# Kernel tuning notes

Hardware: AMD Instinct MI355X
Metric: run time of the kernel (lower is better)

Reference implementation:

```python
import jax, jax.numpy as jnp
import numpy as np

BETA = 0.25

def _encoder(x, W0, b0, W1, b1, W2, b2):
    # MLP: Linear+ReLU, Linear+ReLU, Linear (dims 768->512->256->64)
    h = jax.nn.relu(x @ W0 + b0)
    h = jax.nn.relu(h @ W1 + b1)
    return h @ W2 + b2

def _rvq(z, codebooks):
    # Residual vector quantization over L=4 levels (structurally distinct loop).
    residual = z
    x_q = jnp.zeros_like(z)
    losses = []
    codes = []
    for l in range(codebooks.shape[0]):
        cb = codebooks[l]  # [K, e]
        # squared L2 distances [N, K] via expansion (avoids materializing [N,K,e])
        d = (jnp.sum(residual * residual, axis=1, keepdims=True)
             - 2.0 * residual @ cb.T
             + jnp.sum(cb * cb, axis=1))
        idx = jnp.argmin(d, axis=1)           # [N]
        q = cb[idx]                            # gather [N, e]
        # codebook loss + beta * commitment loss
        loss = (jnp.mean((jax.lax.stop_gradient(q) - residual) ** 2)
                + BETA * jnp.mean((q - jax.lax.stop_gradient(residual)) ** 2))
        losses.append(loss)
        # straight-through estimator
        q_st = residual + jax.lax.stop_gradient(q - residual)
        residual = residual - q_st
        x_q = x_q + q_st
        codes.append(idx)
    rq_loss = jnp.mean(jnp.stack(losses))
    return x_q, rq_loss, jnp.stack(codes)  # codes: [L, N] int


def setup_inputs() -> dict:
    key = jax.random.key(0)
    ks = jax.random.split(key, 8)
    N, D = 131072, 768
    dims = [768, 512, 256, 64]
    x = jax.random.normal(ks[0], (N, D), dtype=jnp.float32)
    W0 = jax.random.normal(ks[1], (dims[0], dims[1]), dtype=jnp.float32) * (1.0 / np.sqrt(dims[0]))
    b0 = jnp.zeros((dims[1],), dtype=jnp.float32)
    W1 = jax.random.normal(ks[2], (dims[1], dims[2]), dtype=jnp.float32) * (1.0 / np.sqrt(dims[1]))
    b1 = jnp.zeros((dims[2],), dtype=jnp.float32)
    W2 = jax.random.normal(ks[3], (dims[2], dims[3]), dtype=jnp.float32) * (1.0 / np.sqrt(dims[2]))
    b2 = jnp.zeros((dims[3],), dtype=jnp.float32)
    codebooks = jax.random.normal(ks[4], (4, 256, 64), dtype=jnp.float32)
    return {"x": x, "W0": W0, "b0": b0, "W1": W1, "b1": b1, "W2": W2, "b2": b2,
            "codebooks": codebooks}


def reference(x, W0, b0, W1, b1, W2, b2, codebooks):
    z = _encoder(x, W0, b0, W1, b1, W2, b2)          # [N, 64]
    x_q, rq_loss, codes = _rvq(z, codebooks)
    return x_q, rq_loss, codes
```

## Files before the change

### kernel.cpp

```cpp
#include <hip/hip_runtime.h>
#include <hip/hip_bf16.h>


typedef double d2v __attribute__((ext_vector_type(2)));

template<bool RELU>
__global__ __launch_bounds__(256) void gemm128(
    const float* __restrict__ A, const float* __restrict__ W,
    const float* __restrict__ bias, float* __restrict__ C,
    int M, int N, int K)
{
    __shared__ float As[16][132];
    __shared__ float Bs[16][132];

    const int tid = threadIdx.x;
    const int tx = tid & 15;
    const int ty = tid >> 4;
    const int col0 = blockIdx.x * 128;
    const int row0 = blockIdx.y * 128;

    const float* Ab = A + (size_t)row0 * K;
    const float* Wb = W + col0;

    const int am0 = tid >> 2,          ak0 = (tid & 3) * 4;
    const int am1 = (tid + 256) >> 2,  ak1 = ((tid + 256) & 3) * 4;
    const int bk0 = tid >> 5,          bn0 = (tid & 31) * 4;
    const int bk1 = (tid + 256) >> 5,  bn1 = ((tid + 256) & 31) * 4;

    float acc[8][8] = {};

    float4 sa0 = *reinterpret_cast<const float4*>(Ab + (size_t)am0 * K + ak0);
    float4 sa1 = *reinterpret_cast<const float4*>(Ab + (size_t)am1 * K + ak1);
    float4 sb0 = *reinterpret_cast<const float4*>(Wb + (size_t)bk0 * N + bn0);
    float4 sb1 = *reinterpret_cast<const float4*>(Wb + (size_t)bk1 * N + bn1);
    As[ak0 + 0][am0] = sa0.x; As[ak0 + 1][am0] = sa0.y;
    As[ak0 + 2][am0] = sa0.z; As[ak0 + 3][am0] = sa0.w;
    As[ak1 + 0][am1] = sa1.x; As[ak1 + 1][am1] = sa1.y;
    As[ak1 + 2][am1] = sa1.z; As[ak1 + 3][am1] = sa1.w;
    *reinterpret_cast<float4*>(&Bs[bk0][bn0]) = sb0;
    *reinterpret_cast<float4*>(&Bs[bk1][bn1]) = sb1;
    __syncthreads();

    for (int k0 = 0; k0 < K; k0 += 16) {
        const bool hasNext = (k0 + 16 < K);
        if (hasNext) {
            const float* An = Ab + k0 + 16;
            const float* Wn = Wb + (size_t)(k0 + 16) * N;
            sa0 = *reinterpret_cast<const float4*>(An + (size_t)am0 * K + ak0);
            sa1 = *reinterpret_cast<const float4*>(An + (size_t)am1 * K + ak1);
            sb0 = *reinterpret_cast<const float4*>(Wn + (size_t)bk0 * N + bn0);
            sb1 = *reinterpret_cast<const float4*>(Wn + (size_t)bk1 * N + bn1);
        }

#pragma unroll
        for (int kk = 0; kk < 16; ++kk) {
            float4 a0 = *reinterpret_cast<const float4*>(&As[kk][ty * 4]);
            float4 a1 = *reinterpret_cast<const float4*>(&As[kk][64 + ty * 4]);
            float4 b0 = *reinterpret_cast<const float4*>(&Bs[kk][tx * 4]);
            float4 b1 = *reinterpret_cast<const float4*>(&Bs[kk][64 + tx * 4]);
            float ar[8] = {a0.x, a0.y, a0.z, a0.w, a1.x, a1.y, a1.z, a1.w};
            float br[8] = {b0.x, b0.y, b0.z, b0.w, b1.x, b1.y, b1.z, b1.w};
#pragma unroll
            for (int m = 0; m < 8; ++m)
#pragma unroll
                for (int n = 0; n < 8; ++n)
                    acc[m][n] = fmaf(ar[m], br[n], acc[m][n]);
        }

        if (hasNext) {
            __syncthreads();
            As[ak0 + 0][am0] = sa0.x; As[ak0 + 1][am0] = sa0.y;
            As[ak0 + 2][am0] = sa0.z; As[ak0 + 3][am0] = sa0.w;
            As[ak1 + 0][am1] = sa1.x; As[ak1 + 1][am1] = sa1.y;
            As[ak1 + 2][am1] = sa1.z; As[ak1 + 3][am1] = sa1.w;
            *reinterpret_cast<float4*>(&Bs[bk0][bn0]) = sb0;
            *reinterpret_cast<float4*>(&Bs[bk1][bn1]) = sb1;
            __syncthreads();
        }
    }

    float bl[4], bh[4];
#pragma unroll
    for (int n = 0; n < 4; ++n) {
        bl[n] = bias[col0 + tx * 4 + n];
        bh[n] = bias[col0 + 64 + tx * 4 + n];
    }
#pragma unroll
    for (int half = 0; half < 2; ++half) {
#pragma unroll
        for (int r = 0; r < 4; ++r) {
            int m = half * 4 + r;
            int row = row0 + half * 64 + ty * 4 + r;
            float4 lo, hi;
            lo.x = acc[m][0] + bl[0]; lo.y = acc[m][1] + bl[1];
            lo.z = acc[m][2] + bl[2]; lo.w = acc[m][3] + bl[3];
            hi.x = acc[m][4] + bh[0]; hi.y = acc[m][5] + bh[1];
            hi.z = acc[m][6] + bh[2]; hi.w = acc[m][7] + bh[3];
            if (RELU) {
                lo.x = fmaxf(lo.x, 0.f); lo.y = fmaxf(lo.y, 0.f);
                lo.z = fmaxf(lo.z, 0.f); lo.w = fmaxf(lo.w, 0.f);
                hi.x = fmaxf(hi.x, 0.f); hi.y = fmaxf(hi.y, 0.f);
                hi.z = fmaxf(hi.z, 0.f); hi.w = fmaxf(hi.w, 0.f);
            }
            float* Cr = C + (size_t)row * N + col0;
            *reinterpret_cast<float4*>(Cr + tx * 4) = lo;
            *reinterpret_cast<float4*>(Cr + 64 + tx * 4) = hi;
        }
    }
}

template<bool RELU>
__global__ __launch_bounds__(256) void gemm_bias(
    const float* __restrict__ A, const float* __restrict__ W,
    const float* __restrict__ bias, float* __restrict__ C,
    int M, int N, int K)
{
    __shared__ float As[16][132];
    __shared__ float Bs[16][68];

    const int tid = threadIdx.x;
    const int tx = tid & 15;
    const int ty = tid >> 4;
    const int col0 = blockIdx.x * 64;
    const int row0 = blockIdx.y * 128;

    const float* Ab = A + (size_t)row0 * K;
    const float* Wb = W + col0;

    float acc[8][4] = {};

    for (int k0 = 0; k0 < K; k0 += 16) {
#pragma unroll
        for (int i = 0; i < 2; ++i) {
            int pos = tid + i * 256;
            int m  = pos >> 2;
            int k4 = (pos & 3) * 4;
            float4 v = *reinterpret_cast<const float4*>(Ab + (size_t)m * K + k0 + k4);
            As[k4 + 0][m] = v.x; As[k4 + 1][m] = v.y;
            As[k4 + 2][m] = v.z; As[k4 + 3][m] = v.w;
        }
        {
            int kk = tid >> 4;
            int n4 = (tid & 15) * 4;
            float4 v = *reinterpret_cast<const float4*>(Wb + (size_t)(k0 + kk) * N + n4);
            *reinterpret_cast<float4*>(&Bs[kk][n4]) = v;
        }
        __syncthreads();
#pragma unroll
        for (int kk = 0; kk < 16; ++kk) {
            float4 a0 = *reinterpret_cast<const float4*>(&As[kk][ty * 8]);
            float4 a1 = *reinterpret_cast<const float4*>(&As[kk][ty * 8 + 4]);
            float4 bv = *reinterpret_cast<const float4*>(&Bs[kk][tx * 4]);
            float a[8] = {a0.x, a0.y, a0.z, a0.w, a1.x, a1.y, a1.z, a1.w};
            float b[4] = {bv.x, bv.y, bv.z, bv.w};
#pragma unroll
            for (int m = 0; m < 8; ++m)
#pragma unroll
                for (int n = 0; n < 4; ++n)
                    acc[m][n] = fmaf(a[m], b[n], acc[m][n]);
        }
        __syncthreads();
    }

    float bv[4];
#pragma unroll
    for (int n = 0; n < 4; ++n) bv[n] = bias[col0 + tx * 4 + n];
#pragma unroll
    for (int m = 0; m < 8; ++m) {
        int row = row0 + ty * 8 + m;
        float4 o;
        float v0 = acc[m][0] + bv[0];
        float v1 = acc[m][1] + bv[1];
        float v2 = acc[m][2] + bv[2];
        float v3 = acc[m][3] + bv[3];
        if (RELU) {
            v0 = fmaxf(v0, 0.f); v1 = fmaxf(v1, 0.f);
            v2 = fmaxf(v2, 0.f); v3 = fmaxf(v3, 0.f);
        }
        o.x = v0; o.y = v1; o.z = v2; o.w = v3;
        *reinterpret_cast<float4*>(C + (size_t)row * N + col0 + tx * 4) = o;
    }
}

__global__ void cb_norms(const float* __restrict__ cb,
                         double* __restrict__ cn64, float* __restrict__ cnf) {
    int c = blockIdx.x * 64 + threadIdx.x;
    const float* p = cb + (size_t)c * 64;
    double s = 0.0;
#pragma unroll
    for (int j = 0; j < 64; ++j) {
        double v = (double)p[j];
        s = fma(v, v, s);
    }
    cn64[c] = s;
    cnf[c]  = (float)s;
}

__global__ void build_cbw(const float* __restrict__ cb, double* __restrict__ cbw) {
    int i = blockIdx.x * 256 + threadIdx.x;
    cbw[i] = -2.0 * (double)cb[i];
}

#define EGUARD 1e-3

__device__ __forceinline__ double rank64(const double* __restrict__ p,
                                         double R0, const float (&rd)[64]) {
    double c0 = 0.0, c1 = 0.0, c2 = 0.0, c3 = 0.0;
#pragma unroll
    for (int j = 0; j < 16; ++j) {
        d2v x = *reinterpret_cast<const d2v*>(p + j * 4);
        d2v y = *reinterpret_cast<const d2v*>(p + j * 4 + 2);
        c0 = fma(x[0], (double)rd[j * 4 + 0], c0);
        c1 = fma(x[1], (double)rd[j * 4 + 1], c1);
        c2 = fma(y[0], (double)rd[j * 4 + 2], c2);
        c3 = fma(y[1], (double)rd[j * 4 + 3], c3);
    }
    return R0 + ((c0 + c1) + (c2 + c3));
}

__global__ __launch_bounds__(256, 2) void rvq_v5(
    const float* __restrict__ z,
    const float* __restrict__ cbf,
    const double* __restrict__ cbw,
    const double* __restrict__ cn64,
    const float* __restrict__ cnf,
    float* __restrict__ xq,
    float* __restrict__ codes,
    double* __restrict__ partials,
    int row0, int Ntot)
{
    __shared__ float sd1[4][64];
    __shared__ float sd2[4][64];
    __shared__ int   si1[4][64];
    __shared__ int   si2[4][64];

    const int tid  = threadIdx.x;
    const int lane = tid & 63;
    const int w    = tid >> 6;
    const int wu   = __builtin_amdgcn_readfirstlane(w);
    const int blk  = blockIdx.x;
    const int grow0 = row0 + blk * 64;

    float rd[64];
    const float* zr = z + (size_t)(blk * 64 + lane) * 64;
#pragma unroll
    for (int q = 0; q < 16; ++q) {
        float4 v = *reinterpret_cast<const float4*>(zr + q * 4);
        rd[q * 4 + 0] = v.x; rd[q * 4 + 1] = v.y;
        rd[q * 4 + 2] = v.z; rd[q * 4 + 3] = v.w;
    }

    double sse = 0.0;

    for (int lv = 0; lv < 4; ++lv) {
        const int cbase = lv * 256;
        __syncthreads();

        const float* cwl = cbf + (size_t)(cbase + wu * 64) * 64;
        const float* cnl = cnf + cbase + wu * 64;

        float d1 = 3.4e38f, d2 = 3.4e38f;
        int   i1 = 0,       i2 = 0;

#pragma unroll 1
        for (int c = 0; c < 64; ++c) {
            const float* cp = cwl + c * 64;
            float acc8[8];
#pragma unroll
            for (int q = 0; q < 8; ++q) {
                float4 va = *reinterpret_cast<const float4*>(cp + q * 8);
                float4 vb = *reinterpret_cast<const float4*>(cp + q * 8 + 4);
                float t = 0.f;
                t = fmaf(va.x, rd[q * 8 + 0], t);
                t = fmaf(va.y, rd[q * 8 + 1], t);
                t = fmaf(va.z, rd[q * 8 + 2], t);
                t = fmaf(va.w, rd[q * 8 + 3], t);
                t = fmaf(vb.x, rd[q * 8 + 4], t);
                t = fmaf(vb.y, rd[q * 8 + 5], t);
                t = fmaf(vb.z, rd[q * 8 + 6], t);
                t = fmaf(vb.w, rd[q * 8 + 7], t);
                acc8[q] = t;
            }
            float dot = ((acc8[0] + acc8[1]) + (acc8[2] + acc8[3]))
                      + ((acc8[4] + acc8[5]) + (acc8[6] + acc8[7]));
            float d = fmaf(-2.f, dot, cnl[c]);
            int code = wu * 64 + c;
            if (d < d1) { d2 = d1; i2 = i1; d1 = d; i1 = code; }
            else if (d < d2) { d2 = d; i2 = code; }
        }

        sd1[w][lane] = d1; si1[w][lane] = i1;
        sd2[w][lane] = d2; si2[w][lane] = i2;
        __syncthreads();

        float bd1 = sd1[0][lane]; int bi1 = si1[0][lane]; int wstar = 0;
#pragma unroll
        for (int ww = 1; ww < 4; ++ww) {
            float dd = sd1[ww][lane]; int ii = si1[ww][lane];
            if (dd < bd1 || (dd == bd1 && ii < bi1)) { bd1 = dd; bi1 = ii; wstar = ww; }
        }
        float d2g = 3.4e38f; int i2g = 0;
#pragma unroll
        for (int ww = 0; ww < 4; ++ww) {
            float dd = (ww == wstar) ? sd2[ww][lane] : sd1[ww][lane];
            int   ii = (ww == wstar) ? si2[ww][lane] : si1[ww][lane];
            if (dd < d2g) { d2g = dd; i2g = ii; }
        }

        double R1 = rank64(cbw + (size_t)(cbase + bi1) * 64, cn64[cbase + bi1], rd);
        double R2 = rank64(cbw + (size_t)(cbase + i2g) * 64, cn64[cbase + i2g], rd);
        int ci; double Rw;
        if (R1 < R2 || (R1 == R2 && bi1 < i2g)) { ci = bi1; Rw = R1; }
        else                                    { ci = i2g; Rw = R2; }

        if (!(Rw < (double)d2g - EGUARD)) {
            float l8f = fminf(fminf(sd2[0][lane], sd2[1][lane]),
                              fminf(sd2[2][lane], sd2[3][lane]));
            double L8 = (double)l8f;
            double Rm = 1.0e300; int im = 0;
#pragma unroll
            for (int ww = 0; ww < 4; ++ww) {
#pragma unroll
                for (int k = 0; k < 2; ++k) {
                    int cc = k ? si2[ww][lane] : si1[ww][lane];
                    double R = rank64(cbw + (size_t)(cbase + cc) * 64,
                                      cn64[cbase + cc], rd);
                    if (R < Rm || (R == Rm && cc < im)) { Rm = R; im = cc; }
                }
            }
            if (Rm < L8 - EGUARD) {
                ci = im;
            } else {
                double dmin = 1.0e300; int imin = 0;
#pragma unroll 1
                for (int c = 0; c < 256; ++c) {
                    double R = rank64(cbw + (size_t)(cbase + c) * 64,
                                      cn64[cbase + c], rd);
                    if (R < dmin) { dmin = R; imin = c; }
                }
                ci = imin;
            }
        }

        const float* qp = cbf + (size_t)(cbase + ci) * 64;
        double lsse = 0.0;
#pragma unroll
        for (int q = 0; q < 16; ++q) {
            float4 qv = *reinterpret_cast<const float4*>(qp + q * 4);
            float r0 = rd[q * 4 + 0], r1 = rd[q * 4 + 1];
            float r2 = rd[q * 4 + 2], r3 = rd[q * 4 + 3];
            if (w == 0) {
                float e0 = qv.x - r0, e1 = qv.y - r1;
                float e2 = qv.z - r2, e3 = qv.w - r3;
                lsse = fma((double)e0, (double)e0, lsse);
                lsse = fma((double)e1, (double)e1, lsse);
                lsse = fma((double)e2, (double)e2, lsse);
                lsse = fma((double)e3, (double)e3, lsse);
            }
            rd[q * 4 + 0] = r0 - qv.x; rd[q * 4 + 1] = r1 - qv.y;
            rd[q * 4 + 2] = r2 - qv.z; rd[q * 4 + 3] = r3 - qv.w;
        }
        if (w == 0) {
            sse += lsse;
            codes[(size_t)lv * Ntot + grow0 + lane] = (float)ci;
        }
    }

    if (w == 0) {
        size_t base = (size_t)(grow0 + lane) * 64;
#pragma unroll
        for (int q = 0; q < 16; ++q) {
            float4 zv = *reinterpret_cast<const float4*>(zr + q * 4);
            float4 o;
            o.x = zv.x - rd[q * 4 + 0];
            o.y = zv.y - rd[q * 4 + 1];
            o.z = zv.z - rd[q * 4 + 2];
            o.w = zv.w - rd[q * 4 + 3];
            *reinterpret_cast<float4*>(xq + base + q * 4) = o;
        }
        double s = sse;
#pragma unroll
        for (int off = 32; off > 0; off >>= 1) {
            union { double d; int i[2]; } u; u.d = s;
            u.i[0] = __shfl_down(u.i[0], off, 64);
            u.i[1] = __shfl_down(u.i[1], off, 64);
            s += u.d;
        }
        if (lane == 0) partials[grow0 >> 6] = s;
    }
}

__global__ void loss_final(const double* __restrict__ partials, int n,
                           float* __restrict__ out, double scale) {
    __shared__ double s[256];
    double acc = 0.0;
    for (int i = threadIdx.x; i < n; i += 256) acc += partials[i];
    s[threadIdx.x] = acc;
    __syncthreads();
    for (int off = 128; off > 0; off >>= 1) {
        if ((int)threadIdx.x < off) s[threadIdx.x] += s[threadIdx.x + off];
        __syncthreads();
    }
    if (threadIdx.x == 0) *out = (float)(s[0] * scale);
}

extern "C" void kernel_launch(void* const* d_in, const int* in_sizes, int n_in,
                              void* d_out, int out_size, void* d_ws, size_t ws_size,
                              hipStream_t stream) {
    const float* x  = (const float*)d_in[0];
    const float* W0 = (const float*)d_in[1];
    const float* b0 = (const float*)d_in[2];
    const float* W1 = (const float*)d_in[3];
    const float* b1 = (const float*)d_in[4];
    const float* W2 = (const float*)d_in[5];
    const float* b2 = (const float*)d_in[6];
    const float* cb = (const float*)d_in[7];

    const int N = in_sizes[0] / 768;

    float* out   = (float*)d_out;
    float* xq    = out;
    float* loss  = out + (size_t)N * 64;
    float* codes = loss + 1;

    const int nblk_total = N / 64;
    const size_t tail_floats = 131072 + 2048 + 2 * (size_t)nblk_total + 1024 + 64;

    size_t avail = ws_size / 4;
    avail = (avail > tail_floats) ? (avail - tail_floats) : 0;
    int Nc = (int)(avail / 832);
    Nc = (Nc / 128) * 128;
    if (Nc > N) Nc = N;
    if (Nc < 128) Nc = 128;

    float* ws = (float*)d_ws;
    float* h0 = ws;
    float* h1 = h0 + (size_t)Nc * 512;
    float* z  = h1 + (size_t)Nc * 256;
    double* cbw      = (double*)(ws + (size_t)Nc * 832);
    double* cn64     = cbw + 65536;
    double* partials = cn64 + 1024;
    float*  cnf      = (float*)(partials + nblk_total);

    cb_norms <<<16, 64, 0, stream>>>(cb, cn64, cnf);
    build_cbw<<<256, 256, 0, stream>>>(cb, cbw);

    for (int r0 = 0; r0 < N; r0 += Nc) {
        int cur = (N - r0 < Nc) ? (N - r0) : Nc;
        gemm128<true ><<<dim3(512 / 128, cur / 128), 256, 0, stream>>>(
            x + (size_t)r0 * 768, W0, b0, h0, cur, 512, 768);
        gemm128<true ><<<dim3(256 / 128, cur / 128), 256, 0, stream>>>(
            h0, W1, b1, h1, cur, 256, 512);
        gemm_bias<false><<<dim3(1, cur / 128), 256, 0, stream>>>(
            h1, W2, b2, z, cur, 64, 256);
        rvq_v5<<<cur / 64, 256, 0, stream>>>(
            z, cb, cbw, cn64, cnf, xq, codes, partials, r0, N);
    }

    loss_final<<<1, 256, 0, stream>>>(partials, nblk_total, loss,
                                      1.25 / (4.0 * (double)N * 64.0));
}
```

Measured before the change: 2.668 ms.

## Double-buffer GEMM shared tiles, remap workgroups per XCD, relax RVQ launch bounds

The fp32 SIMT GEMM now keeps two shared-memory buffers, so the next K tile is written to the spare buffer and only one barrier per step is needed instead of two. Workgroups use a 1D grid whose block ids are remapped so that consecutive tiles land on the same XCD, which is meant to improve L2 reuse of the A rows and weight columns. The RVQ kernel drops its min-blocks-per-CU hint, giving the compiler more registers at the risk of lower occupancy. Doubling the shared tiles also raises LDS use per block.

```diff
diff --git a/kernel.cpp b/kernel.cpp
--- a/kernel.cpp
+++ b/kernel.cpp
@@ -4,20 +4,29 @@
 
 typedef double d2v __attribute__((ext_vector_type(2)));
 
-template<bool RELU>
+template<bool RELU, int NCOLSHIFT>
 __global__ __launch_bounds__(256) void gemm128(
     const float* __restrict__ A, const float* __restrict__ W,
     const float* __restrict__ bias, float* __restrict__ C,
     int M, int N, int K)
 {
-    __shared__ float As[16][132];
-    __shared__ float Bs[16][132];
+    __shared__ float As[2][16][132];
+    __shared__ float Bs[2][16][132];
+
+    const int nwg  = gridDim.x;
+    const int b    = blockIdx.x;
+    const int xcd  = b & 7;
+    const int rest = b >> 3;
+    const int q8   = nwg >> 3, r8 = nwg & 7;
+    const int wg   = (xcd < r8 ? xcd * (q8 + 1) : r8 * (q8 + 1) + (xcd - r8) * q8) + rest;
+    const int NCOL = 1 << NCOLSHIFT;
+
+    const int col0 = (wg & (NCOL - 1)) * 128;
+    const int row0 = (wg >> NCOLSHIFT) * 128;
 
     const int tid = threadIdx.x;
     const int tx = tid & 15;
     const int ty = tid >> 4;
-    const int col0 = blockIdx.x * 128;
-    const int row0 = blockIdx.y * 128;
 
     const float* Ab = A + (size_t)row0 * K;
     const float* Wb = W + col0;
@@ -29,20 +38,24 @@
 
     float acc[8][8] = {};
 
-    float4 sa0 = *reinterpret_cast<const float4*>(Ab + (size_t)am0 * K + ak0);
-    float4 sa1 = *reinterpret_cast<const float4*>(Ab + (size_t)am1 * K + ak1);
-    float4 sb0 = *reinterpret_cast<const float4*>(Wb + (size_t)bk0 * N + bn0);
-    float4 sb1 = *reinterpret_cast<const float4*>(Wb + (size_t)bk1 * N + bn1);
-    As[ak0 + 0][am0] = sa0.x; As[ak0 + 1][am0] = sa0.y;
-    As[ak0 + 2][am0] = sa0.z; As[ak0 + 3][am0] = sa0.w;
-    As[ak1 + 0][am1] = sa1.x; As[ak1 + 1][am1] = sa1.y;
-    As[ak1 + 2][am1] = sa1.z; As[ak1 + 3][am1] = sa1.w;
-    *reinterpret_cast<float4*>(&Bs[bk0][bn0]) = sb0;
-    *reinterpret_cast<float4*>(&Bs[bk1][bn1]) = sb1;
+    {
+        float4 pa0 = *reinterpret_cast<const float4*>(Ab + (size_t)am0 * K + ak0);
+        float4 pa1 = *reinterpret_cast<const float4*>(Ab + (size_t)am1 * K + ak1);
+        float4 pb0 = *reinterpret_cast<const float4*>(Wb + (size_t)bk0 * N + bn0);
+        float4 pb1 = *reinterpret_cast<const float4*>(Wb + (size_t)bk1 * N + bn1);
+        As[0][ak0 + 0][am0] = pa0.x; As[0][ak0 + 1][am0] = pa0.y;
+        As[0][ak0 + 2][am0] = pa0.z; As[0][ak0 + 3][am0] = pa0.w;
+        As[0][ak1 + 0][am1] = pa1.x; As[0][ak1 + 1][am1] = pa1.y;
+        As[0][ak1 + 2][am1] = pa1.z; As[0][ak1 + 3][am1] = pa1.w;
+        *reinterpret_cast<float4*>(&Bs[0][bk0][bn0]) = pb0;
+        *reinterpret_cast<float4*>(&Bs[0][bk1][bn1]) = pb1;
+    }
     __syncthreads();
 
+    int cur = 0;
     for (int k0 = 0; k0 < K; k0 += 16) {
         const bool hasNext = (k0 + 16 < K);
+        float4 sa0, sa1, sb0, sb1;
         if (hasNext) {
             const float* An = Ab + k0 + 16;
             const float* Wn = Wb + (size_t)(k0 + 16) * N;
@@ -54,10 +67,10 @@
 
 #pragma unroll
         for (int kk = 0; kk < 16; ++kk) {
-            float4 a0 = *reinterpret_cast<const float4*>(&As[kk][ty * 4]);
-            float4 a1 = *reinterpret_cast<const float4*>(&As[kk][64 + ty * 4]);
-            float4 b0 = *reinterpret_cast<const float4*>(&Bs[kk][tx * 4]);
-            float4 b1 = *reinterpret_cast<const float4*>(&Bs[kk][64 + tx * 4]);
+            float4 a0 = *reinterpret_cast<const float4*>(&As[cur][kk][ty * 4]);
+            float4 a1 = *reinterpret_cast<const float4*>(&As[cur][kk][64 + ty * 4]);
+            float4 b0 = *reinterpret_cast<const float4*>(&Bs[cur][kk][tx * 4]);
+            float4 b1 = *reinterpret_cast<const float4*>(&Bs[cur][kk][64 + tx * 4]);
             float ar[8] = {a0.x, a0.y, a0.z, a0.w, a1.x, a1.y, a1.z, a1.w};
             float br[8] = {b0.x, b0.y, b0.z, b0.w, b1.x, b1.y, b1.z, b1.w};
 #pragma unroll
@@ -68,14 +81,15 @@
         }
 
         if (hasNext) {
+            int nxt = cur ^ 1;
+            As[nxt][ak0 + 0][am0] = sa0.x; As[nxt][ak0 + 1][am0] = sa0.y;
+            As[nxt][ak0 + 2][am0] = sa0.z; As[nxt][ak0 + 3][am0] = sa0.w;
+            As[nxt][ak1 + 0][am1] = sa1.x; As[nxt][ak1 + 1][am1] = sa1.y;
+            As[nxt][ak1 + 2][am1] = sa1.z; As[nxt][ak1 + 3][am1] = sa1.w;
+            *reinterpret_cast<float4*>(&Bs[nxt][bk0][bn0]) = sb0;
+            *reinterpret_cast<float4*>(&Bs[nxt][bk1][bn1]) = sb1;
             __syncthreads();
-            As[ak0 + 0][am0] = sa0.x; As[ak0 + 1][am0] = sa0.y;
-            As[ak0 + 2][am0] = sa0.z; As[ak0 + 3][am0] = sa0.w;
-            As[ak1 + 0][am1] = sa1.x; As[ak1 + 1][am1] = sa1.y;
-            As[ak1 + 2][am1] = sa1.z; As[ak1 + 3][am1] = sa1.w;
-            *reinterpret_cast<float4*>(&Bs[bk0][bn0]) = sb0;
-            *reinterpret_cast<float4*>(&Bs[bk1][bn1]) = sb1;
-            __syncthreads();
+            cur = nxt;
         }
     }
 
@@ -218,7 +232,7 @@
     return R0 + ((c0 + c1) + (c2 + c3));
 }
 
-__global__ __launch_bounds__(256, 2) void rvq_v5(
+__global__ __launch_bounds__(256) void rvq_v5(
     const float* __restrict__ z,
     const float* __restrict__ cbf,
     const double* __restrict__ cbw,
@@ -447,9 +461,9 @@
 
     for (int r0 = 0; r0 < N; r0 += Nc) {
         int cur = (N - r0 < Nc) ? (N - r0) : Nc;
-        gemm128<true ><<<dim3(512 / 128, cur / 128), 256, 0, stream>>>(
+        gemm128<true, 2><<<4 * (cur / 128), 256, 0, stream>>>(
             x + (size_t)r0 * 768, W0, b0, h0, cur, 512, 768);
-        gemm128<true ><<<dim3(256 / 128, cur / 128), 256, 0, stream>>>(
+        gemm128<true, 1><<<2 * (cur / 128), 256, 0, stream>>>(
             h0, W1, b1, h1, cur, 256, 512);
         gemm_bias<false><<<dim3(1, cur / 128), 256, 0, stream>>>(
             h1, W2, b2, z, cur, 64, 256);
```

Result: slower. 2.999 ms (+12.4%).
